# Performance work log

Hardware: AMD Instinct MI355X
Metric: run time of the kernel (lower is better)

The kernel has to match this reference:

```python
import jax, jax.numpy as jnp
import numpy as np

B, L, D, E, H = 8, 2048, 1024, 8, 2048


def setup_inputs() -> dict:
    key = jax.random.key(0)
    ks = jax.random.split(key, 5)
    scale_in = 1.0 / np.sqrt(D)
    scale_h = 1.0 / np.sqrt(H)
    return {
        "x": jax.random.normal(ks[0], (B, L, D), dtype=jnp.float32),
        "Wg": jax.random.normal(ks[1], (D, E), dtype=jnp.float32) * scale_in,
        "bg": jnp.zeros((E,), dtype=jnp.float32),
        "W1": jax.random.normal(ks[2], (E, D, H), dtype=jnp.float32) * scale_in,
        "b1": jnp.zeros((E, H), dtype=jnp.float32),
        "W2": jax.random.normal(ks[3], (E, H, D), dtype=jnp.float32) * scale_h,
        "b2": jnp.zeros((E, D), dtype=jnp.float32),
    }


def reference(x, Wg, bg, W1, b1, W2, b2):
    # x: [B, L, D] -> tokens [N, D]
    Bs, Ls, Ds = x.shape
    x_flat = x.reshape(-1, Ds)                                   # [N, D]
    gate_logits = x_flat @ Wg + bg                               # [N, E]
    gate_weights = jax.nn.softmax(gate_logits, axis=-1)          # [N, E]
    # top-1 gate (torch.topk with k=1)
    top_idx = jnp.argmax(gate_weights, axis=-1)                  # [N]
    top_w = jnp.max(gate_weights, axis=-1)                       # [N]
    # dense all-expert compute (matches torch.stack over experts)
    hidden = jax.nn.relu(jnp.einsum('nd,edh->neh', x_flat, W1) + b1)  # [N, E, H]
    expert_outputs = jnp.einsum('neh,ehd->ned', hidden, W2) + b2     # [N, E, D]
    # gather the selected expert per token, scale by its gate weight
    selected = jnp.take_along_axis(expert_outputs, top_idx[:, None, None], axis=1)[:, 0, :]  # [N, D]
    out_flat = top_w[:, None] * selected                          # [N, D]
    out = out_flat.reshape(Bs, Ls, Ds)
    return out, gate_weights
```

## Files before the change

### kernel.cpp

```cpp
#include <hip/hip_runtime.h>
#include <hip/hip_bf16.h>

#define N_TOK 16384
#define D_DIM 1024
#define E_NUM 8
#define H_DIM 2048
#define MT 32
#define FFN_BLK 512

typedef __attribute__((ext_vector_type(8))) short short8;
typedef __attribute__((ext_vector_type(4))) float floatx4;

__device__ __forceinline__ unsigned short f2bf_bits(float f) {
    __hip_bfloat16 h = __float2bfloat16(f);
    return *reinterpret_cast<unsigned short*>(&h);
}

__device__ __forceinline__ void async16(const void* g, void* l) {
    __builtin_amdgcn_global_load_lds(
        (const __attribute__((address_space(1))) unsigned int*)g,
        (__attribute__((address_space(3))) unsigned int*)l,
        16, 0, 0);
}

__global__ __launch_bounds__(256) void moe_gate_transpose_fused(
    const float* __restrict__ x,
    const float* __restrict__ Wg,
    const float* __restrict__ bg,
    float* __restrict__ gw_out,
    float* __restrict__ topw,
    int* __restrict__ topidx,
    const float* __restrict__ W1,
    const float* __restrict__ W2,
    unsigned short* __restrict__ W1t,
    unsigned short* __restrict__ W2t) {

    __shared__ float tile[64][65];

    if (blockIdx.x < 8192) {
        int id = blockIdx.x;
        const float* in; unsigned short* out; int R, C, cx, ry, e;
        if (id < 4096) {
            e = id >> 9; int t = id & 511;
            in = W1; out = W1t; R = 1024; C = 2048;
            cx = t & 31; ry = t >> 5;
        } else {
            id -= 4096;
            e = id >> 9; int t = id & 511;
            in = W2; out = W2t; R = 2048; C = 1024;
            cx = t & 15; ry = t >> 4;
        }
        const float* inE = in + (size_t)e * 2097152;
        unsigned short* outE = out + (size_t)e * 2097152;
        int c0 = cx << 6, r0 = ry << 6;
        int tr = threadIdx.x >> 4;
        int tc = (threadIdx.x & 15) << 2;
#pragma unroll
        for (int i = 0; i < 4; i++) {
            int r = tr + (i << 4);
            float4 v = *(const float4*)(inE + (size_t)(r0 + r) * C + c0 + tc);
            tile[r][tc + 0] = v.x; tile[r][tc + 1] = v.y;
            tile[r][tc + 2] = v.z; tile[r][tc + 3] = v.w;
        }
        __syncthreads();
#pragma unroll
        for (int it = 0; it < 2; it++) {
            int task = threadIdx.x + (it << 8);
            int c = task >> 3, rr = (task & 7) << 3;
            short8 o;
#pragma unroll
            for (int j = 0; j < 8; j++)
                ((unsigned short*)&o)[j] = f2bf_bits(tile[rr + j][c]);
            *(short8*)(outE + (size_t)(c0 + c) * R + r0 + rr) = o;
        }
        return;
    }

    int bid = blockIdx.x - 8192;
    int wave = ((bid << 8) + threadIdx.x) >> 6;
    int lane = threadIdx.x & 63;
    if (wave >= N_TOK) return;
    const float* xr = x + (size_t)wave * D_DIM;

    float4 xv[4];
#pragma unroll
    for (int i = 0; i < 4; i++)
        xv[i] = *(const float4*)(xr + i * 256 + lane * 4);

    float acc[8];
#pragma unroll
    for (int e = 0; e < 8; e++) acc[e] = 0.f;

#pragma unroll
    for (int i = 0; i < 4; i++) {
        const float xs4[4] = {xv[i].x, xv[i].y, xv[i].z, xv[i].w};
        const float* wp = Wg + ((size_t)(i * 256) + lane * 4) * 8;
#pragma unroll
        for (int j = 0; j < 4; j++) {
            float4 w0 = *(const float4*)(wp + j * 8);
            float4 w1 = *(const float4*)(wp + j * 8 + 4);
            float s = xs4[j];
            acc[0] += s * w0.x; acc[1] += s * w0.y;
            acc[2] += s * w0.z; acc[3] += s * w0.w;
            acc[4] += s * w1.x; acc[5] += s * w1.y;
            acc[6] += s * w1.z; acc[7] += s * w1.w;
        }
    }
#pragma unroll
    for (int e = 0; e < 8; e++) {
#pragma unroll
        for (int off = 32; off > 0; off >>= 1)
            acc[e] += __shfl_xor(acc[e], off, 64);
    }
#pragma unroll
    for (int e = 0; e < 8; e++) acc[e] += bg[e];

    float mx = acc[0]; int am = 0;
#pragma unroll
    for (int e = 1; e < 8; e++) { if (acc[e] > mx) { mx = acc[e]; am = e; } }
    float w[8], s = 0.f;
#pragma unroll
    for (int e = 0; e < 8; e++) { w[e] = expf(acc[e] - mx); s += w[e]; }
    float inv = 1.f / s;
#pragma unroll
    for (int e = 0; e < 8; e++) w[e] *= inv;

    if (lane == 0) {
        float4 a = make_float4(w[0], w[1], w[2], w[3]);
        float4 b = make_float4(w[4], w[5], w[6], w[7]);
        *(float4*)(gw_out + (size_t)wave * 8)     = a;
        *(float4*)(gw_out + (size_t)wave * 8 + 4) = b;
        topw[wave]   = w[am];
        topidx[wave] = am;
    }
}

__global__ __launch_bounds__(256) void moe_gate_kernel(
    const float* __restrict__ x,
    const float* __restrict__ Wg,
    const float* __restrict__ bg,
    float* __restrict__ gw_out,
    float* __restrict__ topw,
    int* __restrict__ topidx) {
    int wave = (blockIdx.x * blockDim.x + threadIdx.x) >> 6;
    int lane = threadIdx.x & 63;
    if (wave >= N_TOK) return;
    const float* xr = x + (size_t)wave * D_DIM;

    float4 xv[4];
#pragma unroll
    for (int i = 0; i < 4; i++)
        xv[i] = *(const float4*)(xr + i * 256 + lane * 4);

    float acc[8];
#pragma unroll
    for (int e = 0; e < 8; e++) acc[e] = 0.f;
#pragma unroll
    for (int i = 0; i < 4; i++) {
        const float xs4[4] = {xv[i].x, xv[i].y, xv[i].z, xv[i].w};
        const float* wp = Wg + ((size_t)(i * 256) + lane * 4) * 8;
#pragma unroll
        for (int j = 0; j < 4; j++) {
            float4 w0 = *(const float4*)(wp + j * 8);
            float4 w1 = *(const float4*)(wp + j * 8 + 4);
            float s = xs4[j];
            acc[0] += s * w0.x; acc[1] += s * w0.y;
            acc[2] += s * w0.z; acc[3] += s * w0.w;
            acc[4] += s * w1.x; acc[5] += s * w1.y;
            acc[6] += s * w1.z; acc[7] += s * w1.w;
        }
    }
#pragma unroll
    for (int e = 0; e < 8; e++) {
#pragma unroll
        for (int off = 32; off > 0; off >>= 1)
            acc[e] += __shfl_xor(acc[e], off, 64);
    }
#pragma unroll
    for (int e = 0; e < 8; e++) acc[e] += bg[e];

    float mx = acc[0]; int am = 0;
#pragma unroll
    for (int e = 1; e < 8; e++) { if (acc[e] > mx) { mx = acc[e]; am = e; } }
    float w[8], s = 0.f;
#pragma unroll
    for (int e = 0; e < 8; e++) { w[e] = expf(acc[e] - mx); s += w[e]; }
    float inv = 1.f / s;
#pragma unroll
    for (int e = 0; e < 8; e++) w[e] *= inv;

    if (lane == 0) {
        float4 a = make_float4(w[0], w[1], w[2], w[3]);
        float4 b = make_float4(w[4], w[5], w[6], w[7]);
        *(float4*)(gw_out + (size_t)wave * 8)     = a;
        *(float4*)(gw_out + (size_t)wave * 8 + 4) = b;
        topw[wave]   = w[am];
        topidx[wave] = am;
    }
}

__global__ __launch_bounds__(256) void moe_hist_scan_kernel(
    const int* __restrict__ topidx,
    int* __restrict__ offsets,
    int* __restrict__ cursor) {
    __shared__ int part[256][8];
    int tid = threadIdx.x;
    int c0 = 0, c1 = 0, c2 = 0, c3 = 0, c4 = 0, c5 = 0, c6 = 0, c7 = 0;
    const int4* tp = (const int4*)topidx;
    for (int i = 0; i < N_TOK / 1024; i++) {
        int4 v = tp[tid + (i << 8)];
#pragma unroll
        for (int j = 0; j < 4; j++) {
            int idx = (&v.x)[j];
            c0 += (idx == 0); c1 += (idx == 1); c2 += (idx == 2); c3 += (idx == 3);
            c4 += (idx == 4); c5 += (idx == 5); c6 += (idx == 6); c7 += (idx == 7);
        }
    }
    part[tid][0] = c0; part[tid][1] = c1; part[tid][2] = c2; part[tid][3] = c3;
    part[tid][4] = c4; part[tid][5] = c5; part[tid][6] = c6; part[tid][7] = c7;
    __syncthreads();
    for (int s = 128; s > 0; s >>= 1) {
        if (tid < s) {
#pragma unroll
            for (int e = 0; e < 8; e++) part[tid][e] += part[tid + s][e];
        }
        __syncthreads();
    }
    if (tid == 0) {
        int run = 0;
        for (int e = 0; e < 8; e++) {
            offsets[e] = run;
            cursor[e]  = run;
            run += part[0][e];
        }
        offsets[8] = run;
    }
}

__global__ __launch_bounds__(256) void moe_scatter_gather(
    const float* __restrict__ x,
    const int* __restrict__ topidx,
    int* __restrict__ cursor,
    int* __restrict__ toksort,
    unsigned short* __restrict__ xs) {
    __shared__ int lcnt[8];
    __shared__ int lbase[8];
    __shared__ int s_pos[64];
    int tid = threadIdx.x;
    int base = blockIdx.x << 6;
    if (tid < 8) lcnt[tid] = 0;
    __syncthreads();
    int e = 0, r = 0;
    if (tid < 64) {
        e = topidx[base + tid];
        r = atomicAdd(&lcnt[e], 1);
    }
    __syncthreads();
    if (tid < 8) lbase[tid] = atomicAdd(&cursor[tid], lcnt[tid]);
    __syncthreads();
    if (tid < 64) {
        int p = lbase[e] + r;
        toksort[p] = base + tid;
        s_pos[tid] = p;
    }
    __syncthreads();
    for (int rr = 0; rr < 64; rr++) {
        int tok = base + rr;
        int p = s_pos[rr];
        float4 v = *(const float4*)(x + (size_t)tok * D_DIM + (tid << 2));
        ushort4 o;
        o.x = f2bf_bits(v.x); o.y = f2bf_bits(v.y);
        o.z = f2bf_bits(v.z); o.w = f2bf_bits(v.w);
        *(ushort4*)(xs + (size_t)p * D_DIM + (tid << 2)) = o;
    }
}

__global__ __launch_bounds__(256) void moe_scatter_kernel(
    const int* __restrict__ topidx,
    int* __restrict__ cursor,
    int* __restrict__ toksort) {
    __shared__ int lcnt[8];
    __shared__ int lbase[8];
    int tid = threadIdx.x;
    int t = blockIdx.x * blockDim.x + tid;
    if (tid < 8) lcnt[tid] = 0;
    __syncthreads();
    int e = topidx[t];
    int r = atomicAdd(&lcnt[e], 1);
    __syncthreads();
    if (tid < 8) lbase[tid] = atomicAdd(&cursor[tid], lcnt[tid]);
    __syncthreads();
    toksort[lbase[e] + r] = t;
}

__device__ __forceinline__ int find_tile(const int* offsets, int mt,
                                         int& row0, int& rows) {
    int cum = 0;
    for (int ee = 0; ee < E_NUM; ee++) {
        int o0 = offsets[ee], o1 = offsets[ee + 1];
        int tiles = (o1 - o0 + 127) >> 7;
        if (mt < cum + tiles) {
            row0 = o0 + ((mt - cum) << 7);
            rows = o1 - row0; if (rows > 128) rows = 128;
            return ee;
        }
        cum += tiles;
    }
    return -1;
}

__device__ __forceinline__ void xcd_swizzle(int& bx, int& by) {
    int nwgx = gridDim.x;
    int id = blockIdx.y * nwgx + blockIdx.x;
    int nwg = nwgx * gridDim.y;
    int cpx = nwg >> 3;
    int swz = (id & 7) * cpx + (id >> 3);
    bx = swz % nwgx; by = swz / nwgx;
}

__global__ __launch_bounds__(256) void moe_ffn1_mfma(
    const unsigned short* __restrict__ xs,
    const unsigned short* __restrict__ W1t,
    const float* __restrict__ b1,
    const int* __restrict__ offsets,
    unsigned short* __restrict__ hb) {

    __shared__ __align__(16) unsigned short LDS[128 * 132];
    unsigned short* As = LDS;
    unsigned short* Bs = LDS + 4096;

    int bx, by;
    xcd_swizzle(bx, by);

    int row0, rows;
    int e = find_tile(offsets, bx, row0, rows);
    if (e < 0) return;
    int n0 = by << 7;

    int tid = threadIdx.x, l = tid & 63, w = tid >> 6;
    int wm = w & 1, wn = w >> 1;
    int lrow = l & 15, lq = l >> 4;
    const unsigned short* Be = W1t + (size_t)e * H_DIM * D_DIM;

    floatx4 acc[4][4];
#pragma unroll
    for (int mi = 0; mi < 4; mi++)
#pragma unroll
        for (int ni = 0; ni < 4; ni++) acc[mi][ni] = floatx4{0.f, 0.f, 0.f, 0.f};

    int srow = (w << 5) + (l >> 2);
    int koff = (l & 3) << 3;

    for (int kt = 0; kt < D_DIM / 32; kt++) {
        int kb = kt << 5;
        __syncthreads();
#pragma unroll
        for (int i = 0; i < 2; i++) {
            int r = srow + (i << 4);
            int p = row0 + r; if (p > N_TOK - 1) p = N_TOK - 1;
            async16(xs + (size_t)p * D_DIM + kb + koff,
                    As + (((w << 5) + (i << 4)) << 5));
            async16(Be + (size_t)(n0 + r) * D_DIM + kb + koff,
                    Bs + (((w << 5) + (i << 4)) << 5));
        }
        __syncthreads();
        short8 af[4], bfv[4];
#pragma unroll
        for (int mi = 0; mi < 4; mi++)
            af[mi] = *(const short8*)(As + (((wm << 6) + (mi << 4) + lrow) << 5) + (lq << 3));
#pragma unroll
        for (int ni = 0; ni < 4; ni++)
            bfv[ni] = *(const short8*)(Bs + (((wn << 6) + (ni << 4) + lrow) << 5) + (lq << 3));
#pragma unroll
        for (int mi = 0; mi < 4; mi++)
#pragma unroll
            for (int ni = 0; ni < 4; ni++)
                acc[mi][ni] = __builtin_amdgcn_mfma_f32_16x16x32_bf16(
                    af[mi], bfv[ni], acc[mi][ni], 0, 0, 0);
    }

    __syncthreads();
#pragma unroll
    for (int ni = 0; ni < 4; ni++) {
        int cl = (wn << 6) + (ni << 4) + lrow;
        float bias = b1[e * H_DIM + n0 + cl];
#pragma unroll
        for (int mi = 0; mi < 4; mi++) {
#pragma unroll
            for (int r = 0; r < 4; r++) {
                int rl = (wm << 6) + (mi << 4) + (lq << 2) + r;
                float v = acc[mi][ni][r] + bias;
                v = v > 0.f ? v : 0.f;
                LDS[rl * 132 + cl] = f2bf_bits(v);
            }
        }
    }
    __syncthreads();
    int trow = tid >> 1, tcol = (tid & 1) << 6;
    if (trow < rows) {
        unsigned short* dst = hb + (size_t)(row0 + trow) * H_DIM + n0 + tcol;
        const unsigned short* src = LDS + trow * 132 + tcol;
#pragma unroll
        for (int i2 = 0; i2 < 8; i2++)
            *(short8*)(dst + i2 * 8) = *(const short8*)(src + i2 * 8);
    }
}

__global__ __launch_bounds__(256) void moe_ffn2_mfma(
    const unsigned short* __restrict__ hb,
    const unsigned short* __restrict__ W2t,
    const float* __restrict__ b2,
    const int* __restrict__ offsets,
    const int* __restrict__ toksort,
    const float* __restrict__ topw,
    float* __restrict__ out) {

    __shared__ __align__(16) unsigned short As[128 * 32];
    __shared__ __align__(16) unsigned short Bs[128 * 32];

    int bx, by;
    xcd_swizzle(bx, by);

    int row0, rows;
    int e = find_tile(offsets, bx, row0, rows);
    if (e < 0) return;
    int n0 = by << 7;

    int tid = threadIdx.x, l = tid & 63, w = tid >> 6;
    int wm = w & 1, wn = w >> 1;
    int lrow = l & 15, lq = l >> 4;
    const unsigned short* Be = W2t + (size_t)e * D_DIM * H_DIM;

    floatx4 acc[4][4];
#pragma unroll
    for (int mi = 0; mi < 4; mi++)
#pragma unroll
        for (int ni = 0; ni < 4; ni++) acc[mi][ni] = floatx4{0.f, 0.f, 0.f, 0.f};

    int srow = (w << 5) + (l >> 2);
    int koff = (l & 3) << 3;

    for (int kt = 0; kt < H_DIM / 32; kt++) {
        int kb = kt << 5;
        __syncthreads();
#pragma unroll
        for (int i = 0; i < 2; i++) {
            int r = srow + (i << 4);
            int p = row0 + r; if (p > N_TOK - 1) p = N_TOK - 1;
            async16(hb + (size_t)p * H_DIM + kb + koff,
                    As + (((w << 5) + (i << 4)) << 5));
            async16(Be + (size_t)(n0 + r) * H_DIM + kb + koff,
                    Bs + (((w << 5) + (i << 4)) << 5));
        }
        __syncthreads();
        short8 af[4], bfv[4];
#pragma unroll
        for (int mi = 0; mi < 4; mi++)
            af[mi] = *(const short8*)(As + (((wm << 6) + (mi << 4) + lrow) << 5) + (lq << 3));
#pragma unroll
        for (int ni = 0; ni < 4; ni++)
            bfv[ni] = *(const short8*)(Bs + (((wn << 6) + (ni << 4) + lrow) << 5) + (lq << 3));
#pragma unroll
        for (int mi = 0; mi < 4; mi++)
#pragma unroll
            for (int ni = 0; ni < 4; ni++)
                acc[mi][ni] = __builtin_amdgcn_mfma_f32_16x16x32_bf16(
                    af[mi], bfv[ni], acc[mi][ni], 0, 0, 0);
    }

    float bias[4];
#pragma unroll
    for (int ni = 0; ni < 4; ni++)
        bias[ni] = b2[e * D_DIM + n0 + (wn << 6) + (ni << 4) + lrow];

#pragma unroll
    for (int mi = 0; mi < 4; mi++) {
#pragma unroll
        for (int r = 0; r < 4; r++) {
            int row = (wm << 6) + (mi << 4) + (lq << 2) + r;
            if (row < rows) {
                int p = row0 + row;
                int tok = toksort[p];
                float tw = topw[tok];
#pragma unroll
                for (int ni = 0; ni < 4; ni++) {
                    int d = n0 + (wn << 6) + (ni << 4) + lrow;
                    out[(size_t)tok * D_DIM + d] = tw * (acc[mi][ni][r] + bias[ni]);
                }
            }
        }
    }
}

__global__ __launch_bounds__(FFN_BLK, 2) void moe_ffn_kernel(
    const float* __restrict__ x,
    const float* __restrict__ W1, const float* __restrict__ b1,
    const float* __restrict__ W2, const float* __restrict__ b2,
    const int* __restrict__ offsets,
    const int* __restrict__ toksort,
    const float* __restrict__ topw,
    float* __restrict__ out) {

    __shared__ __align__(16) unsigned short h1c[MT * 1024];
    float* xs = (float*)h1c;

    int bid = blockIdx.x;
    int e = -1, row0 = 0, rows = 0, cum = 0;
    for (int ee = 0; ee < E_NUM; ee++) {
        int o0 = offsets[ee], o1 = offsets[ee + 1];
        int tiles = (o1 - o0 + MT - 1) / MT;
        if (bid < cum + tiles) {
            e = ee;
            row0 = o0 + (bid - cum) * MT;
            rows = (o1 - row0 < MT) ? (o1 - row0) : MT;
            break;
        }
        cum += tiles;
    }
    if (e < 0) return;

    int tid = threadIdx.x;
    const float* W1e = W1 + (size_t)e * D_DIM * H_DIM;
    const float* W2e = W2 + (size_t)e * H_DIM * D_DIM;

    int m_st = tid >> 4;
    int j_st = tid & 15;
    int m_cl = (m_st < rows) ? m_st : (rows - 1);
    int tok_st = toksort[row0 + m_cl];

    float acc2x[MT], acc2y[MT];
#pragma unroll
    for (int m = 0; m < MT; m++) { acc2x[m] = 0.f; acc2y[m] = 0.f; }

    int d0 = tid * 2;

    for (int half = 0; half < 2; half++) {
        int ha = half * 1024 + tid;
        int hb_ = ha + 512;

        float a1a[MT], a1b[MT];
#pragma unroll
        for (int m = 0; m < MT; m++) { a1a[m] = 0.f; a1b[m] = 0.f; }

        for (int dc = 0; dc < 8; dc++) {
            __syncthreads();
            {
                const float4* src =
                    (const float4*)(x + (size_t)tok_st * D_DIM + dc * 128 + j_st * 8);
                float4 v0 = src[0], v1 = src[1];
                float4* dst = (float4*)(xs + m_st * 128 + j_st * 8);
                dst[0] = v0; dst[1] = v1;
            }
            __syncthreads();
            const float* w1pa = W1e + (size_t)(dc * 128) * H_DIM + ha;
            const float* w1pb = W1e + (size_t)(dc * 128) * H_DIM + hb_;
            for (int d2 = 0; d2 < 64; d2++) {
                float wa0 = w1pa[0], wa1 = w1pa[H_DIM];
                float wb0 = w1pb[0], wb1 = w1pb[H_DIM];
                w1pa += 2 * H_DIM; w1pb += 2 * H_DIM;
#pragma unroll
                for (int m = 0; m < MT; m++) {
                    float2 xv = *(const float2*)(xs + m * 128 + d2 * 2);
                    a1a[m] += xv.x * wa0; a1a[m] += xv.y * wa1;
                    a1b[m] += xv.x * wb0; a1b[m] += xv.y * wb1;
                }
            }
        }

        float bba = b1[e * H_DIM + ha];
        float bbb = b1[e * H_DIM + hb_];
        __syncthreads();
#pragma unroll
        for (int m = 0; m < MT; m++) {
            float va = a1a[m] + bba; va = va > 0.f ? va : 0.f;
            float vb = a1b[m] + bbb; vb = vb > 0.f ? vb : 0.f;
            h1c[m * 1024 + tid]       = f2bf_bits(va);
            h1c[m * 1024 + 512 + tid] = f2bf_bits(vb);
        }
        __syncthreads();

        const float* w2p = W2e + (size_t)(half * 1024) * D_DIM + d0;
        for (int hh = 0; hh < 1024; hh += 2) {
            float2 w2a = *(const float2*)(w2p);
            float2 w2b = *(const float2*)(w2p + D_DIM);
            w2p += 2 * D_DIM;
#pragma unroll
            for (int m = 0; m < MT; m++) {
                unsigned int u = *(const unsigned int*)(h1c + m * 1024 + hh);
                float h0  = __uint_as_float(u << 16);
                float h1v = __uint_as_float(u & 0xffff0000u);
                acc2x[m] += h0 * w2a.x; acc2x[m] += h1v * w2b.x;
                acc2y[m] += h0 * w2a.y; acc2y[m] += h1v * w2b.y;
            }
        }
    }

    float bb0 = b2[e * D_DIM + d0];
    float bb1 = b2[e * D_DIM + d0 + 1];
#pragma unroll
    for (int m = 0; m < MT; m++) {
        if (m < rows) {
            int tok  = toksort[row0 + m];
            float tw = topw[tok];
            float2 o;
            o.x = tw * (acc2x[m] + bb0);
            o.y = tw * (acc2y[m] + bb1);
            *(float2*)(out + (size_t)tok * D_DIM + d0) = o;
        }
    }
}

extern "C" void kernel_launch(void* const* d_in, const int* in_sizes, int n_in,
                              void* d_out, int out_size, void* d_ws, size_t ws_size,
                              hipStream_t stream) {
    const float* x  = (const float*)d_in[0];
    const float* Wg = (const float*)d_in[1];
    const float* bg = (const float*)d_in[2];
    const float* W1 = (const float*)d_in[3];
    const float* b1 = (const float*)d_in[4];
    const float* W2 = (const float*)d_in[5];
    const float* b2 = (const float*)d_in[6];

    float* out = (float*)d_out;
    float* gw  = out + (size_t)N_TOK * D_DIM;

    char* ws = (char*)d_ws;
    int*   counts  = (int*)ws;
    int*   cursor  = counts + 8;
    int*   offsets = cursor + 8;
    int*   topidx  = (int*)(ws + 128);
    float* topw    = (float*)(ws + 128 + 4 * (size_t)N_TOK);
    int*   toksort = (int*)(ws + 128 + 8 * (size_t)N_TOK);

    const size_t off_xs  = 256ull << 10;
    const size_t off_w1t = off_xs  + (32ull << 20);
    const size_t off_w2t = off_w1t + (32ull << 20);
    const size_t off_hb  = off_w2t + (32ull << 20);
    const size_t need    = off_hb  + (64ull << 20);

    if (ws_size >= need) {
        unsigned short* xs  = (unsigned short*)(ws + off_xs);
        unsigned short* W1t = (unsigned short*)(ws + off_w1t);
        unsigned short* W2t = (unsigned short*)(ws + off_w2t);
        unsigned short* hb  = (unsigned short*)(ws + off_hb);

        moe_gate_transpose_fused<<<12288, 256, 0, stream>>>(
            x, Wg, bg, gw, topw, topidx, W1, W2, W1t, W2t);
        moe_hist_scan_kernel<<<1, 256, 0, stream>>>(topidx, offsets, cursor);
        moe_scatter_gather<<<N_TOK / 64, 256, 0, stream>>>(
            x, topidx, cursor, toksort, xs);

        moe_ffn1_mfma<<<dim3(N_TOK / 128 + E_NUM, H_DIM / 128), 256, 0, stream>>>(
            xs, W1t, b1, offsets, hb);
        moe_ffn2_mfma<<<dim3(N_TOK / 128 + E_NUM, D_DIM / 128), 256, 0, stream>>>(
            hb, W2t, b2, offsets, toksort, topw, out);
    } else {
        moe_gate_kernel<<<N_TOK / 4, 256, 0, stream>>>(
            x, Wg, bg, gw, topw, topidx);
        moe_hist_scan_kernel<<<1, 256, 0, stream>>>(topidx, offsets, cursor);
        moe_scatter_kernel<<<N_TOK / 256, 256, 0, stream>>>(topidx, cursor, toksort);
        moe_ffn_kernel<<<N_TOK / MT + E_NUM, FFN_BLK, 0, stream>>>(
            x, W1, b1, W2, b2, offsets, toksort, topw, out);
    }
}
```

Baseline: 533.2 us.

## Fuse bf16 x cast into gate, gather rows in GEMM, use BK=64 swizzled LDS

The gate kernel now also writes a bf16 copy of x. The scatter_gather kernel is replaced by a plain index scatter, and FFN1 gathers token rows through toksort while loading A tiles. Both FFN GEMMs share a helper with a K-tile of 64 instead of 32 and an XOR-swizzled LDS layout, which halves the barriers per K and should cut bank conflicts. The XCD swizzle of block indices is dropped, which may hurt L2 locality of the weight tiles, and the gathered A loads are no longer contiguous.

```diff
diff --git a/kernel.cpp b/kernel.cpp
--- a/kernel.cpp
+++ b/kernel.cpp
@@ -30,6 +30,7 @@
     float* __restrict__ gw_out,
     float* __restrict__ topw,
     int* __restrict__ topidx,
+    unsigned short* __restrict__ xb,
     const float* __restrict__ W1,
     const float* __restrict__ W2,
     unsigned short* __restrict__ W1t,
@@ -87,6 +88,14 @@
     for (int i = 0; i < 4; i++)
         xv[i] = *(const float4*)(xr + i * 256 + lane * 4);
 
+#pragma unroll
+    for (int i = 0; i < 4; i++) {
+        ushort4 o;
+        o.x = f2bf_bits(xv[i].x); o.y = f2bf_bits(xv[i].y);
+        o.z = f2bf_bits(xv[i].z); o.w = f2bf_bits(xv[i].w);
+        *(ushort4*)(xb + (size_t)wave * D_DIM + i * 256 + lane * 4) = o;
+    }
+
     float acc[8];
 #pragma unroll
     for (int e = 0; e < 8; e++) acc[e] = 0.f;
@@ -234,44 +243,6 @@
             run += part[0][e];
         }
         offsets[8] = run;
-    }
-}
-
-__global__ __launch_bounds__(256) void moe_scatter_gather(
-    const float* __restrict__ x,
-    const int* __restrict__ topidx,
-    int* __restrict__ cursor,
-    int* __restrict__ toksort,
-    unsigned short* __restrict__ xs) {
-    __shared__ int lcnt[8];
-    __shared__ int lbase[8];
-    __shared__ int s_pos[64];
-    int tid = threadIdx.x;
-    int base = blockIdx.x << 6;
-    if (tid < 8) lcnt[tid] = 0;
-    __syncthreads();
-    int e = 0, r = 0;
-    if (tid < 64) {
-        e = topidx[base + tid];
-        r = atomicAdd(&lcnt[e], 1);
-    }
-    __syncthreads();
-    if (tid < 8) lbase[tid] = atomicAdd(&cursor[tid], lcnt[tid]);
-    __syncthreads();
-    if (tid < 64) {
-        int p = lbase[e] + r;
-        toksort[p] = base + tid;
-        s_pos[tid] = p;
-    }
-    __syncthreads();
-    for (int rr = 0; rr < 64; rr++) {
-        int tok = base + rr;
-        int p = s_pos[rr];
-        float4 v = *(const float4*)(x + (size_t)tok * D_DIM + (tid << 2));
-        ushort4 o;
-        o.x = f2bf_bits(v.x); o.y = f2bf_bits(v.y);
-        o.z = f2bf_bits(v.z); o.w = f2bf_bits(v.w);
-        *(ushort4*)(xs + (size_t)p * D_DIM + (tid << 2)) = o;
     }
 }
 
@@ -309,17 +280,72 @@
     return -1;
 }
 
-__device__ __forceinline__ void xcd_swizzle(int& bx, int& by) {
-    int nwgx = gridDim.x;
-    int id = blockIdx.y * nwgx + blockIdx.x;
-    int nwg = nwgx * gridDim.y;
-    int cpx = nwg >> 3;
-    int swz = (id & 7) * cpx + (id >> 3);
-    bx = swz % nwgx; by = swz / nwgx;
+template<int LDK, bool GATHER>
+__device__ __forceinline__ void gemm128_bk64(
+    const unsigned short* __restrict__ Ag,
+    const int* __restrict__ toksort,
+    const unsigned short* __restrict__ Be,
+    int row0, int n0,
+    unsigned short* As, unsigned short* Bs,
+    floatx4 (&acc)[4][4]) {
+
+    const int tid = threadIdx.x;
+    const int l = tid & 63, w = tid >> 6;
+    const int wm = w & 1, wn = w >> 1;
+    const int lrow = l & 15, lq = l >> 4;
+    const int r8 = l >> 3;
+    const int g  = l & 7;
+    const int kg = ((g ^ r8) & 7) << 3;
+
+    const unsigned short* aptr[4];
+    const unsigned short* bptr[4];
+#pragma unroll
+    for (int j = 0; j < 4; j++) {
+        int r = j * 32 + w * 8 + r8;
+        int p = row0 + r; if (p > N_TOK - 1) p = N_TOK - 1;
+        if (GATHER) p = toksort[p];
+        aptr[j] = Ag + (size_t)p * LDK + kg;
+        bptr[j] = Be + (size_t)(n0 + r) * LDK + kg;
+    }
+
+    const int xora = (lrow & 7);
+
+    for (int kt = 0; kt < LDK / 64; kt++) {
+        const int kb = kt << 6;
+        __syncthreads();
+#pragma unroll
+        for (int j = 0; j < 4; j++) {
+            async16(aptr[j] + kb, As + ((j * 32 + w * 8) << 6));
+            async16(bptr[j] + kb, Bs + ((j * 32 + w * 8) << 6));
+        }
+        __syncthreads();
+#pragma unroll
+        for (int kk = 0; kk < 2; kk++) {
+            short8 af[4], bfv[4];
+            const int gl = ((kk << 2) + lq) ^ xora;
+#pragma unroll
+            for (int mi = 0; mi < 4; mi++) {
+                int row = (wm << 6) + (mi << 4) + lrow;
+                af[mi] = *(const short8*)(As + (row << 6) + (gl << 3));
+            }
+#pragma unroll
+            for (int ni = 0; ni < 4; ni++) {
+                int row = (wn << 6) + (ni << 4) + lrow;
+                bfv[ni] = *(const short8*)(Bs + (row << 6) + (gl << 3));
+            }
+#pragma unroll
+            for (int mi = 0; mi < 4; mi++)
+#pragma unroll
+                for (int ni = 0; ni < 4; ni++)
+                    acc[mi][ni] = __builtin_amdgcn_mfma_f32_16x16x32_bf16(
+                        af[mi], bfv[ni], acc[mi][ni], 0, 0, 0);
+        }
+    }
 }
 
 __global__ __launch_bounds__(256) void moe_ffn1_mfma(
-    const unsigned short* __restrict__ xs,
+    const unsigned short* __restrict__ xb,
+    const int* __restrict__ toksort,
     const unsigned short* __restrict__ W1t,
     const float* __restrict__ b1,
     const int* __restrict__ offsets,
@@ -327,20 +353,16 @@
 
     __shared__ __align__(16) unsigned short LDS[128 * 132];
     unsigned short* As = LDS;
-    unsigned short* Bs = LDS + 4096;
-
-    int bx, by;
-    xcd_swizzle(bx, by);
+    unsigned short* Bs = LDS + 8192;
 
     int row0, rows;
-    int e = find_tile(offsets, bx, row0, rows);
+    int e = find_tile(offsets, blockIdx.x, row0, rows);
     if (e < 0) return;
-    int n0 = by << 7;
+    int n0 = blockIdx.y << 7;
 
     int tid = threadIdx.x, l = tid & 63, w = tid >> 6;
     int wm = w & 1, wn = w >> 1;
     int lrow = l & 15, lq = l >> 4;
-    const unsigned short* Be = W1t + (size_t)e * H_DIM * D_DIM;
 
     floatx4 acc[4][4];
 #pragma unroll
@@ -348,36 +370,8 @@
 #pragma unroll
         for (int ni = 0; ni < 4; ni++) acc[mi][ni] = floatx4{0.f, 0.f, 0.f, 0.f};
 
-    int srow = (w << 5) + (l >> 2);
-    int koff = (l & 3) << 3;
-
-    for (int kt = 0; kt < D_DIM / 32; kt++) {
-        int kb = kt << 5;
-        __syncthreads();
-#pragma unroll
-        for (int i = 0; i < 2; i++) {
-            int r = srow + (i << 4);
-            int p = row0 + r; if (p > N_TOK - 1) p = N_TOK - 1;
-            async16(xs + (size_t)p * D_DIM + kb + koff,
-                    As + (((w << 5) + (i << 4)) << 5));
-            async16(Be + (size_t)(n0 + r) * D_DIM + kb + koff,
-                    Bs + (((w << 5) + (i << 4)) << 5));
-        }
-        __syncthreads();
-        short8 af[4], bfv[4];
-#pragma unroll
-        for (int mi = 0; mi < 4; mi++)
-            af[mi] = *(const short8*)(As + (((wm << 6) + (mi << 4) + lrow) << 5) + (lq << 3));
-#pragma unroll
-        for (int ni = 0; ni < 4; ni++)
-            bfv[ni] = *(const short8*)(Bs + (((wn << 6) + (ni << 4) + lrow) << 5) + (lq << 3));
-#pragma unroll
-        for (int mi = 0; mi < 4; mi++)
-#pragma unroll
-            for (int ni = 0; ni < 4; ni++)
-                acc[mi][ni] = __builtin_amdgcn_mfma_f32_16x16x32_bf16(
-                    af[mi], bfv[ni], acc[mi][ni], 0, 0, 0);
-    }
+    gemm128_bk64<D_DIM, true>(xb, toksort, W1t + (size_t)e * H_DIM * D_DIM,
+                              row0, n0, As, Bs, acc);
 
     __syncthreads();
 #pragma unroll
@@ -415,21 +409,17 @@
     const float* __restrict__ topw,
     float* __restrict__ out) {
 
-    __shared__ __align__(16) unsigned short As[128 * 32];
-    __shared__ __align__(16) unsigned short Bs[128 * 32];
-
-    int bx, by;
-    xcd_swizzle(bx, by);
+    __shared__ __align__(16) unsigned short As[128 * 64];
+    __shared__ __align__(16) unsigned short Bs[128 * 64];
 
     int row0, rows;
-    int e = find_tile(offsets, bx, row0, rows);
+    int e = find_tile(offsets, blockIdx.x, row0, rows);
     if (e < 0) return;
-    int n0 = by << 7;
+    int n0 = blockIdx.y << 7;
 
     int tid = threadIdx.x, l = tid & 63, w = tid >> 6;
     int wm = w & 1, wn = w >> 1;
     int lrow = l & 15, lq = l >> 4;
-    const unsigned short* Be = W2t + (size_t)e * D_DIM * H_DIM;
 
     floatx4 acc[4][4];
 #pragma unroll
@@ -437,36 +427,8 @@
 #pragma unroll
         for (int ni = 0; ni < 4; ni++) acc[mi][ni] = floatx4{0.f, 0.f, 0.f, 0.f};
 
-    int srow = (w << 5) + (l >> 2);
-    int koff = (l & 3) << 3;
-
-    for (int kt = 0; kt < H_DIM / 32; kt++) {
-        int kb = kt << 5;
-        __syncthreads();
-#pragma unroll
-        for (int i = 0; i < 2; i++) {
-            int r = srow + (i << 4);
-            int p = row0 + r; if (p > N_TOK - 1) p = N_TOK - 1;
-            async16(hb + (size_t)p * H_DIM + kb + koff,
-                    As + (((w << 5) + (i << 4)) << 5));
-            async16(Be + (size_t)(n0 + r) * H_DIM + kb + koff,
-                    Bs + (((w << 5) + (i << 4)) << 5));
-        }
-        __syncthreads();
-        short8 af[4], bfv[4];
-#pragma unroll
-        for (int mi = 0; mi < 4; mi++)
-            af[mi] = *(const short8*)(As + (((wm << 6) + (mi << 4) + lrow) << 5) + (lq << 3));
-#pragma unroll
-        for (int ni = 0; ni < 4; ni++)
-            bfv[ni] = *(const short8*)(Bs + (((wn << 6) + (ni << 4) + lrow) << 5) + (lq << 3));
-#pragma unroll
-        for (int mi = 0; mi < 4; mi++)
-#pragma unroll
-            for (int ni = 0; ni < 4; ni++)
-                acc[mi][ni] = __builtin_amdgcn_mfma_f32_16x16x32_bf16(
-                    af[mi], bfv[ni], acc[mi][ni], 0, 0, 0);
-    }
+    gemm128_bk64<H_DIM, false>(hb, toksort, W2t + (size_t)e * D_DIM * H_DIM,
+                               row0, n0, As, Bs, acc);
 
     float bias[4];
 #pragma unroll
@@ -632,26 +594,25 @@
     float* topw    = (float*)(ws + 128 + 4 * (size_t)N_TOK);
     int*   toksort = (int*)(ws + 128 + 8 * (size_t)N_TOK);
 
-    const size_t off_xs  = 256ull << 10;
-    const size_t off_w1t = off_xs  + (32ull << 20);
+    const size_t off_xb  = 256ull << 10;
+    const size_t off_w1t = off_xb  + (32ull << 20);
     const size_t off_w2t = off_w1t + (32ull << 20);
     const size_t off_hb  = off_w2t + (32ull << 20);
     const size_t need    = off_hb  + (64ull << 20);
 
     if (ws_size >= need) {
-        unsigned short* xs  = (unsigned short*)(ws + off_xs);
+        unsigned short* xb  = (unsigned short*)(ws + off_xb);
         unsigned short* W1t = (unsigned short*)(ws + off_w1t);
         unsigned short* W2t = (unsigned short*)(ws + off_w2t);
         unsigned short* hb  = (unsigned short*)(ws + off_hb);
 
         moe_gate_transpose_fused<<<12288, 256, 0, stream>>>(
-            x, Wg, bg, gw, topw, topidx, W1, W2, W1t, W2t);
+            x, Wg, bg, gw, topw, topidx, xb, W1, W2, W1t, W2t);
         moe_hist_scan_kernel<<<1, 256, 0, stream>>>(topidx, offsets, cursor);
-        moe_scatter_gather<<<N_TOK / 64, 256, 0, stream>>>(
-            x, topidx, cursor, toksort, xs);
+        moe_scatter_kernel<<<N_TOK / 256, 256, 0, stream>>>(topidx, cursor, toksort);
 
         moe_ffn1_mfma<<<dim3(N_TOK / 128 + E_NUM, H_DIM / 128), 256, 0, stream>>>(
-            xs, W1t, b1, offsets, hb);
+            xb, toksort, W1t, b1, offsets, hb);
         moe_ffn2_mfma<<<dim3(N_TOK / 128 + E_NUM, D_DIM / 128), 256, 0, stream>>>(
             hb, W2t, b2, offsets, toksort, topw, out);
     } else {
```

New measurement: 542.1 us. About the same (+1.7%).
